# Kernel tuning notes

Hardware: AMD Instinct MI355X
Metric: run time of the kernel (lower is better)

The kernel has to match this reference:

```python
import jax, jax.numpy as jnp
import numpy as np

C, H, W = 64, 282, 282
PILLAR_SIZE = 0.16
RANGE_MIN = -22.0


def _scatter_forward(PFN_input, PFN_output):
    # PFN_input: [B, 2, P, 1] pillar (x, y) coords; PFN_output: [B, C, P] features
    x = PFN_input[:, 0, :, 0]  # [B, P]
    y = PFN_input[:, 1, :, 0]  # [B, P]
    valid = x != 0  # original uses nonzero(PFN_input[b,0,:,0]) as pillar list
    # digitize into grid cells (equivalent of get_grid over arange(-22,22,0.16))
    xg = jnp.floor((x - RANGE_MIN) / PILLAR_SIZE).astype(jnp.int32)
    yg = jnp.floor((y - RANGE_MIN) / PILLAR_SIZE).astype(jnp.int32)
    # route invalid pillars to an out-of-bounds index; jax scatter drops OOB updates
    xg = jnp.where(valid, jnp.clip(xg, 0, W - 1), W)
    yg = jnp.where(valid, jnp.clip(yg, 0, H - 1), H)

    def scatter_one(xgb, ygb, feats):  # xgb,ygb: [P]; feats: [C, P]
        canvas = jnp.zeros((C, H, W), feats.dtype)
        return canvas.at[:, ygb, xgb].set(feats)

    return jax.vmap(scatter_one)(xg, yg, PFN_output)  # [B, C, H, W]


def setup_inputs() -> dict:
    key = jax.random.key(0)
    k1, k2 = jax.random.split(key)
    B, P = 4, 12000
    PFN_input = jax.random.uniform(k1, (B, 2, P, 1), dtype=jnp.float32,
                                   minval=-22.0, maxval=22.0)
    PFN_output = jax.random.normal(k2, (B, C, P), dtype=jnp.float32)
    return {"PFN_input": PFN_input, "PFN_output": PFN_output}


def reference(PFN_input, PFN_output):
    return _scatter_forward(PFN_input, PFN_output)
```

## Files before the change

### kernel.cpp

```cpp
#include <hip/hip_runtime.h>

#define NB 4
#define NC 64
#define NH 282
#define NW 282
#define NP 12000
#define HWC (NH * NW)
#define QHW (HWC / 4)
#define CLAIM_INTS (NB * HWC)
#define QCHUNK 64
#define NQBLK ((QHW + QCHUNK - 1) / QCHUNK)
#define NBLKS (8 * NQBLK)

__device__ __align__(16) int g_claim[CLAIM_INTS];

__global__ void pps_claim_kernel(const float* __restrict__ pfn_in) {
    int gid = blockIdx.x * blockDim.x + threadIdx.x;
    if (gid >= NB * NP) return;
    int b = gid / NP;
    int p = gid - b * NP;
    const float* base = pfn_in + (size_t)b * 2 * NP;
    float x = base[p];
    if (x == 0.0f) return;
    float y = base[NP + p];
    int xg = (int)floorf((x + 22.0f) * 6.25f);
    int yg = (int)floorf((y + 22.0f) * 6.25f);
    xg = min(max(xg, 0), NW - 1);
    yg = min(max(yg, 0), NH - 1);
    atomicMax(&g_claim[b * HWC + yg * NW + xg], p + 1);
}

__global__ __launch_bounds__(256) void pps_fill6_kernel(
        const float* __restrict__ pfn_out, float4* __restrict__ out) {
    const int bid = blockIdx.x;
    const int slot = bid & 7;
    const int rest = bid >> 3;
    const int b = slot >> 1;
    const int ch0 = (slot & 1) * 32;
    const int lane = threadIdx.x & 63;
    const int cg = threadIdx.x >> 6;
    const int q = rest * QCHUNK + lane;

    int4 c4 = make_int4(0, 0, 0, 0);
    if (q < QHW) c4 = ((const int4*)(g_claim + b * HWC))[q];

    const float* rowbase = pfn_out + ((size_t)b * NC + ch0 + cg * 8) * NP;
    float4* dst = out + ((size_t)b * NC + ch0 + cg * 8) * QHW + q;

    #pragma unroll
    for (int cc = 0; cc < 8; ++cc) {
        const float* row = rowbase + (size_t)cc * NP;
        float4 v;
        v.x = (c4.x > 0) ? row[c4.x - 1] : 0.0f;
        v.y = (c4.y > 0) ? row[c4.y - 1] : 0.0f;
        v.z = (c4.z > 0) ? row[c4.z - 1] : 0.0f;
        v.w = (c4.w > 0) ? row[c4.w - 1] : 0.0f;
        if (q < QHW) dst[(size_t)cc * QHW] = v;
    }
}

extern "C" void kernel_launch(void* const* d_in, const int* in_sizes, int n_in,
                              void* d_out, int out_size, void* d_ws, size_t ws_size,
                              hipStream_t stream) {
    const float* pfn_in  = (const float*)d_in[0];
    const float* pfn_out = (const float*)d_in[1];
    float4* out = (float4*)d_out;
    (void)d_ws; (void)ws_size;

    {
        int total = NB * NP;
        pps_claim_kernel<<<(total + 255) / 256, 256, 0, stream>>>(pfn_in);
    }
    {
        pps_fill6_kernel<<<NBLKS, 256, 0, stream>>>(pfn_out, out);
    }
}
```

Measured before the change: 110.9 us.

## Transpose pillar features to point-major layout for contiguous per-cell gathers

Adds a prepass that transposes PFN_output from [B,C,P] to [B,P,C] in workspace memory through a shared-memory tile. The same launch also runs the claim atomics in extra blocks, merging the two prepass launches into one. The fill kernel then loads 8 contiguous channels per claimed cell with two float4 reads instead of 8 strided scalar gathers, aiming to cut scattered memory traffic. The cost is an extra write and read of the feature tensor, plus reliance on workspace size.

Result: no change. 109.1 us (median of 2 runs) (-1.7%).

```diff
diff --git a/kernel.cpp b/kernel.cpp
--- a/kernel.cpp
+++ b/kernel.cpp
@@ -11,27 +11,57 @@
 #define QCHUNK 64
 #define NQBLK ((QHW + QCHUNK - 1) / QCHUNK)
 #define NBLKS (8 * NQBLK)
+#define PTILE 64
+#define NPT ((NP + PTILE - 1) / PTILE)
+#define TR_BLOCKS (NB * NPT)
+#define CL_BLOCKS 188
 
 __device__ __align__(16) int g_claim[CLAIM_INTS];
 
-__global__ void pps_claim_kernel(const float* __restrict__ pfn_in) {
-    int gid = blockIdx.x * blockDim.x + threadIdx.x;
-    if (gid >= NB * NP) return;
-    int b = gid / NP;
-    int p = gid - b * NP;
-    const float* base = pfn_in + (size_t)b * 2 * NP;
-    float x = base[p];
-    if (x == 0.0f) return;
-    float y = base[NP + p];
-    int xg = (int)floorf((x + 22.0f) * 6.25f);
-    int yg = (int)floorf((y + 22.0f) * 6.25f);
-    xg = min(max(xg, 0), NW - 1);
-    yg = min(max(yg, 0), NH - 1);
-    atomicMax(&g_claim[b * HWC + yg * NW + xg], p + 1);
+__global__ __launch_bounds__(256) void pps_prepass_kernel(
+        const float* __restrict__ pfn_in,
+        const float* __restrict__ pfn_out,
+        float* __restrict__ T) {
+    __shared__ float tile[PTILE][PTILE + 1];
+    const int bid = blockIdx.x;
+    if (bid < TR_BLOCKS) {
+        const int b = bid / NPT;
+        const int p0 = (bid - b * NPT) * PTILE;
+        const int px = threadIdx.x & 63;
+        const int cy = threadIdx.x >> 6;
+        const float* src = pfn_out + (size_t)b * NC * NP;
+        #pragma unroll
+        for (int i = 0; i < 16; ++i) {
+            int c = cy + i * 4;
+            int p = p0 + px;
+            tile[px][c] = (p < NP) ? src[(size_t)c * NP + p] : 0.0f;
+        }
+        __syncthreads();
+        float* dstb = T + ((size_t)b * NP + p0) * NC;
+        #pragma unroll
+        for (int i = 0; i < 16; ++i) {
+            int pl = cy + i * 4;
+            if (p0 + pl < NP) dstb[(size_t)pl * NC + px] = tile[pl][px];
+        }
+    } else {
+        int gid = (bid - TR_BLOCKS) * 256 + threadIdx.x;
+        if (gid >= NB * NP) return;
+        int b = gid / NP;
+        int p = gid - b * NP;
+        const float* base = pfn_in + (size_t)b * 2 * NP;
+        float x = base[p];
+        if (x == 0.0f) return;
+        float y = base[NP + p];
+        int xg = (int)floorf((x + 22.0f) * 6.25f);
+        int yg = (int)floorf((y + 22.0f) * 6.25f);
+        xg = min(max(xg, 0), NW - 1);
+        yg = min(max(yg, 0), NH - 1);
+        atomicMax(&g_claim[b * HWC + yg * NW + xg], p + 1);
+    }
 }
 
-__global__ __launch_bounds__(256) void pps_fill6_kernel(
-        const float* __restrict__ pfn_out, float4* __restrict__ out) {
+__global__ __launch_bounds__(256) void pps_fill7_kernel(
+        const float* __restrict__ T, float4* __restrict__ out) {
     const int bid = blockIdx.x;
     const int slot = bid & 7;
     const int rest = bid >> 3;
@@ -44,18 +74,38 @@
     int4 c4 = make_int4(0, 0, 0, 0);
     if (q < QHW) c4 = ((const int4*)(g_claim + b * HWC))[q];
 
-    const float* rowbase = pfn_out + ((size_t)b * NC + ch0 + cg * 8) * NP;
-    float4* dst = out + ((size_t)b * NC + ch0 + cg * 8) * QHW + q;
+    float a0[8], a1[8], a2[8], a3[8];
+    #pragma unroll
+    for (int k = 0; k < 8; ++k) { a0[k] = 0.0f; a1[k] = 0.0f; a2[k] = 0.0f; a3[k] = 0.0f; }
+    const int coff = ch0 + cg * 8;
+    if (c4.x > 0) {
+        const float4* s = (const float4*)(T + (((size_t)b * NP + (c4.x - 1)) << 6) + coff);
+        float4 u = s[0], w = s[1];
+        a0[0]=u.x; a0[1]=u.y; a0[2]=u.z; a0[3]=u.w; a0[4]=w.x; a0[5]=w.y; a0[6]=w.z; a0[7]=w.w;
+    }
+    if (c4.y > 0) {
+        const float4* s = (const float4*)(T + (((size_t)b * NP + (c4.y - 1)) << 6) + coff);
+        float4 u = s[0], w = s[1];
+        a1[0]=u.x; a1[1]=u.y; a1[2]=u.z; a1[3]=u.w; a1[4]=w.x; a1[5]=w.y; a1[6]=w.z; a1[7]=w.w;
+    }
+    if (c4.z > 0) {
+        const float4* s = (const float4*)(T + (((size_t)b * NP + (c4.z - 1)) << 6) + coff);
+        float4 u = s[0], w = s[1];
+        a2[0]=u.x; a2[1]=u.y; a2[2]=u.z; a2[3]=u.w; a2[4]=w.x; a2[5]=w.y; a2[6]=w.z; a2[7]=w.w;
+    }
+    if (c4.w > 0) {
+        const float4* s = (const float4*)(T + (((size_t)b * NP + (c4.w - 1)) << 6) + coff);
+        float4 u = s[0], w = s[1];
+        a3[0]=u.x; a3[1]=u.y; a3[2]=u.z; a3[3]=u.w; a3[4]=w.x; a3[5]=w.y; a3[6]=w.z; a3[7]=w.w;
+    }
 
-    #pragma unroll
-    for (int cc = 0; cc < 8; ++cc) {
-        const float* row = rowbase + (size_t)cc * NP;
-        float4 v;
-        v.x = (c4.x > 0) ? row[c4.x - 1] : 0.0f;
-        v.y = (c4.y > 0) ? row[c4.y - 1] : 0.0f;
-        v.z = (c4.z > 0) ? row[c4.z - 1] : 0.0f;
-        v.w = (c4.w > 0) ? row[c4.w - 1] : 0.0f;
-        if (q < QHW) dst[(size_t)cc * QHW] = v;
+    float4* dst = out + ((size_t)b * NC + coff) * QHW + q;
+    if (q < QHW) {
+        #pragma unroll
+        for (int cc = 0; cc < 8; ++cc) {
+            float4 v = make_float4(a0[cc], a1[cc], a2[cc], a3[cc]);
+            dst[(size_t)cc * QHW] = v;
+        }
     }
 }
 
@@ -65,13 +115,8 @@
     const float* pfn_in  = (const float*)d_in[0];
     const float* pfn_out = (const float*)d_in[1];
     float4* out = (float4*)d_out;
-    (void)d_ws; (void)ws_size;
+    float* T = (float*)d_ws;
 
-    {
-        int total = NB * NP;
-        pps_claim_kernel<<<(total + 255) / 256, 256, 0, stream>>>(pfn_in);
-    }
-    {
-        pps_fill6_kernel<<<NBLKS, 256, 0, stream>>>(pfn_out, out);
-    }
+    pps_prepass_kernel<<<TR_BLOCKS + CL_BLOCKS, 256, 0, stream>>>(pfn_in, pfn_out, T);
+    pps_fill7_kernel<<<NBLKS, 256, 0, stream>>>(T, out);
 }
```
